# Performance work log

Measured on AMD Instinct MI355X. Metric: run time of the kernel, lower is better.

Reference implementation:

```python
import jax, jax.numpy as jnp
import numpy as np

E, D, H, T = 8, 2048, 5632, 32768  # experts, dim, hidden_dim, total routed tokens


def setup_inputs() -> dict:
    key = jax.random.key(0)
    k_x, k1, k2, k3 = jax.random.split(key, 4)
    x = jax.random.normal(k_x, (T, D), dtype=jnp.float32)
    # trunc_normal init stds per init_weights (approx: plain normal, same scale)
    std = (2.0 / (D * 24)) ** 0.5
    w1 = jax.random.normal(k1, (E, H, D), dtype=jnp.float32) * std
    w2 = jax.random.normal(k2, (E, D, H), dtype=jnp.float32) * std
    w3 = jax.random.normal(k3, (E, H, D), dtype=jnp.float32) * std
    # tokens are pre-sorted by expert; even split 4096 tokens/expert (sums to T)
    num_tokens_per_expert = jnp.full((E,), T // E, dtype=jnp.int32)
    return {"x": x, "w1": w1, "w2": w2, "w3": w3,
            "num_tokens_per_expert": num_tokens_per_expert}


def _grouped_experts(x, w1, w2, w3, counts):
    # Faithful to _run_experts_grouped_mm: grouped GEMMs computed in bf16,
    # SwiGLU activation, cast back to x dtype.
    xb = x.astype(jnp.bfloat16)
    w1b = jnp.transpose(w1.astype(jnp.bfloat16), (0, 2, 1))  # [E, D, H]
    w3b = jnp.transpose(w3.astype(jnp.bfloat16), (0, 2, 1))  # [E, D, H]
    w2b = jnp.transpose(w2.astype(jnp.bfloat16), (0, 2, 1))  # [E, H, D]
    h1 = jax.lax.ragged_dot(xb, w1b, counts)   # [T, H]
    h3 = jax.lax.ragged_dot(xb, w3b, counts)   # [T, H]
    h = jax.nn.silu(h1) * h3                   # fused SwiGLU gate
    out = jax.lax.ragged_dot(h, w2b, counts)   # [T, D]
    return out.astype(x.dtype)


def reference(x, w1, w2, w3, num_tokens_per_expert):
    return _grouped_experts(x, w1, w2, w3, num_tokens_per_expert)
```

## Files before the change

### kernel.cpp

```cpp
#include <hip/hip_runtime.h>
#include <hip/hip_bf16.h>
#include <stdint.h>

#define TT 32768
#define DD 2048
#define HH 5632
#define NE 8

typedef __bf16 bf16;
typedef __bf16 bf16x8 __attribute__((ext_vector_type(8)));
typedef float  f32x4  __attribute__((ext_vector_type(4)));

__device__ __forceinline__ void gl16(const void* g, void* l) {
    __builtin_amdgcn_global_load_lds(
        (const __attribute__((address_space(1))) void*)g,
        (__attribute__((address_space(3))) void*)l, 16, 0, 0);
}
#define VMW(n) asm volatile("s_waitcnt vmcnt(" #n ")" ::: "memory")
#define LGKM0() do { asm volatile("s_waitcnt lgkmcnt(0)" ::: "memory"); \
                     __builtin_amdgcn_sched_barrier(0); } while (0)
#define BARRIER() __builtin_amdgcn_s_barrier()

__device__ __forceinline__ int swz(int off) { return off ^ (((off >> 7) & 3) << 4); }

__device__ __forceinline__ int expert_of(const int* counts, int row0) {
    int base = 0;
    for (int i = 0; i < NE; ++i) { int c = counts[i]; if (row0 < base + c) return i; base += c; }
    return NE - 1;
}

__global__ __launch_bounds__(256)
void k_cvt(const float* __restrict__ in, bf16* __restrict__ out, long n) {
    long i = ((long)blockIdx.x * 256 + threadIdx.x) * 8;
    const long stride = (long)gridDim.x * 256 * 8;
    for (; i < n; i += stride) {
        const float4* p = (const float4*)(in + i);
        float4 a = p[0], b = p[1];
        union { bf16 v[8]; uint4 u; } r;
        r.v[0] = (bf16)a.x; r.v[1] = (bf16)a.y; r.v[2] = (bf16)a.z; r.v[3] = (bf16)a.w;
        r.v[4] = (bf16)b.x; r.v[5] = (bf16)b.y; r.v[6] = (bf16)b.z; r.v[7] = (bf16)b.w;
        *(uint4*)(out + i) = r.u;
    }
}

__global__ __launch_bounds__(512, 2)
void k_moe1(const bf16* __restrict__ xb, const bf16* __restrict__ w1b,
            const bf16* __restrict__ w3b, const int* __restrict__ counts,
            bf16* __restrict__ h) {
    extern __shared__ __align__(16) char sm[];
    const int tid = threadIdx.x;
    const int nwg = gridDim.x;
    int wg = blockIdx.x;
    wg = (wg & 7) * (nwg >> 3) + (wg >> 3);
    const int NTN = HH / 128;
    const int mt = wg / NTN, nt = wg - mt * NTN;
    const int row0 = mt * 256, col0 = nt * 128;
    const int e = expert_of(counts, row0);

    const char *sa0, *sa1, *sa2, *sa3;
    {
        int off0 = tid * 16, off1 = 8192 + tid * 16;
        int s0 = swz(off0), s1 = swz(off1);
        sa0 = (const char*)xb + (((size_t)(row0 + (s0 >> 6)) * DD) << 1) + (s0 & 63);
        sa1 = (const char*)xb + (((size_t)(row0 + (s1 >> 6)) * DD) << 1) + (s1 & 63);
        const char* w1p = (const char*)(w1b + (size_t)e * HH * DD);
        const char* w3p = (const char*)(w3b + (size_t)e * HH * DD);
        sa2 = w1p + (((size_t)(col0 + (s0 >> 6)) * DD) << 1) + (s0 & 63);
        sa3 = w3p + (((size_t)(col0 + (s0 >> 6)) * DD) << 1) + (s0 & 63);
    }
    const int dst0 = tid * 16;

    auto stageA = [&](int kt) {
        char* db = sm + ((kt & 3) << 15);
        const size_t ko = (size_t)kt << 6;
        gl16(sa0 + ko, db + dst0);
        gl16(sa1 + ko, db + 8192 + dst0);
    };
    auto stageB = [&](int kt) {
        char* db = sm + ((kt & 3) << 15);
        const size_t ko = (size_t)kt << 6;
        gl16(sa2 + ko, db + 16384 + dst0);
        gl16(sa3 + ko, db + 24576 + dst0);
    };

    const int lane = tid & 63, wv = tid >> 6;
    const int wrow = wv >> 2, wcol = wv & 3;
    const int lrow = lane & 15, kb = (lane >> 4) << 4;

    int aoff[8], boff[2];
#pragma unroll
    for (int mi = 0; mi < 8; ++mi) aoff[mi] = swz((wrow * 128 + mi * 16 + lrow) * 64 + kb);
#pragma unroll
    for (int ni = 0; ni < 2; ++ni) boff[ni] = swz((wcol * 32 + ni * 16 + lrow) * 64 + kb);

    f32x4 acc1[8][2] = {};
    f32x4 acc3[8][2] = {};

    const int NT = DD / 32;
    stageA(0); stageB(0); stageA(1); stageB(1); stageA(2); stageB(2);
    VMW(8);
    BARRIER();
    for (int t = 0; t < NT; ++t) {
        const char* db = sm + ((t & 3) << 15);
        bf16x8 b1[2], b3[2];
        {
            bf16x8 af[4];
#pragma unroll
            for (int mi = 0; mi < 4; ++mi) af[mi] = *(const bf16x8*)(db + aoff[mi]);
#pragma unroll
            for (int ni = 0; ni < 2; ++ni) {
                b1[ni] = *(const bf16x8*)(db + 16384 + boff[ni]);
                b3[ni] = *(const bf16x8*)(db + 24576 + boff[ni]);
            }
            if (t + 3 < NT) stageA(t + 3);
            BARRIER();
            LGKM0();
            __builtin_amdgcn_s_setprio(1);
#pragma unroll
            for (int mi = 0; mi < 4; ++mi)
#pragma unroll
                for (int ni = 0; ni < 2; ++ni) {
                    acc1[mi][ni] = __builtin_amdgcn_mfma_f32_16x16x32_bf16(af[mi], b1[ni], acc1[mi][ni], 0, 0, 0);
                    acc3[mi][ni] = __builtin_amdgcn_mfma_f32_16x16x32_bf16(af[mi], b3[ni], acc3[mi][ni], 0, 0, 0);
                }
            __builtin_amdgcn_s_setprio(0);
            BARRIER();
        }
        {
            bf16x8 af[4];
#pragma unroll
            for (int mi = 0; mi < 4; ++mi) af[mi] = *(const bf16x8*)(db + aoff[mi + 4]);
            if (t + 3 < NT) { stageB(t + 3); VMW(8); }
            else if (t == NT - 3) { VMW(4); }
            else if (t == NT - 2) { VMW(0); }
            BARRIER();
            LGKM0();
            __builtin_amdgcn_s_setprio(1);
#pragma unroll
            for (int mi = 0; mi < 4; ++mi)
#pragma unroll
                for (int ni = 0; ni < 2; ++ni) {
                    acc1[mi + 4][ni] = __builtin_amdgcn_mfma_f32_16x16x32_bf16(af[mi], b1[ni], acc1[mi + 4][ni], 0, 0, 0);
                    acc3[mi + 4][ni] = __builtin_amdgcn_mfma_f32_16x16x32_bf16(af[mi], b3[ni], acc3[mi + 4][ni], 0, 0, 0);
                }
            __builtin_amdgcn_s_setprio(0);
            BARRIER();
        }
    }

#pragma unroll
    for (int mi = 0; mi < 8; ++mi)
#pragma unroll
        for (int ni = 0; ni < 2; ++ni)
#pragma unroll
            for (int j = 0; j < 4; ++j) {
                int row = row0 + wrow * 128 + mi * 16 + ((lane >> 4) << 2) + j;
                int col = col0 + wcol * 32 + ni * 16 + lrow;
                float f1 = (float)(bf16)acc1[mi][ni][j];
                float f3 = (float)(bf16)acc3[mi][ni][j];
                float s = f1 / (1.0f + __expf(-f1));
                h[(size_t)row * HH + col] = (bf16)(s * f3);
            }
}

__global__ __launch_bounds__(512, 2)
void k_g2(const bf16* __restrict__ hb, const bf16* __restrict__ w2b,
          const int* __restrict__ counts, float* __restrict__ out) {
    extern __shared__ __align__(16) char sm[];
    const int tid = threadIdx.x;
    const int nwg = gridDim.x;
    int wg = blockIdx.x;
    wg = (wg & 7) * (nwg >> 3) + (wg >> 3);
    const int NTN = DD / 256;
    const int mt = wg / NTN, nt = wg - mt * NTN;
    const int row0 = mt * 256, col0 = nt * 256;
    const int e = expert_of(counts, row0);

    const char *sa0, *sa1, *sa2, *sa3;
    {
        int off0 = tid * 16, off1 = 8192 + tid * 16;
        int s0 = swz(off0), s1 = swz(off1);
        sa0 = (const char*)hb + (((size_t)(row0 + (s0 >> 6)) * HH) << 1) + (s0 & 63);
        sa1 = (const char*)hb + (((size_t)(row0 + (s1 >> 6)) * HH) << 1) + (s1 & 63);
        const char* wp = (const char*)(w2b + (size_t)e * DD * HH);
        sa2 = wp + (((size_t)(col0 + (s0 >> 6)) * HH) << 1) + (s0 & 63);
        sa3 = wp + (((size_t)(col0 + (s1 >> 6)) * HH) << 1) + (s1 & 63);
    }
    const int dst0 = tid * 16;
    auto stageA = [&](int kt) {
        char* db = sm + ((kt & 3) << 15);
        const size_t ko = (size_t)kt << 6;
        gl16(sa0 + ko, db + dst0);
        gl16(sa1 + ko, db + 8192 + dst0);
    };
    auto stageB = [&](int kt) {
        char* db = sm + ((kt & 3) << 15);
        const size_t ko = (size_t)kt << 6;
        gl16(sa2 + ko, db + 16384 + dst0);
        gl16(sa3 + ko, db + 24576 + dst0);
    };

    const int lane = tid & 63, wv = tid >> 6;
    const int wrow = wv >> 2, wcol = wv & 3;
    const int lrow = lane & 15, kb = (lane >> 4) << 4;

    int aoff[8], boff[4];
#pragma unroll
    for (int mi = 0; mi < 8; ++mi) aoff[mi] = swz((wrow * 128 + mi * 16 + lrow) * 64 + kb);
#pragma unroll
    for (int ni = 0; ni < 4; ++ni) boff[ni] = swz((wcol * 64 + ni * 16 + lrow) * 64 + kb);

    f32x4 acc[8][4] = {};
    const int NT = HH / 32;
    stageA(0); stageB(0); stageA(1); stageB(1); stageA(2); stageB(2);
    VMW(8);
    BARRIER();
    for (int t = 0; t < NT; ++t) {
        const char* db = sm + ((t & 3) << 15);
        bf16x8 bf[4];
        {
            bf16x8 af[4];
#pragma unroll
            for (int mi = 0; mi < 4; ++mi) af[mi] = *(const bf16x8*)(db + aoff[mi]);
#pragma unroll
            for (int ni = 0; ni < 4; ++ni) bf[ni] = *(const bf16x8*)(db + 16384 + boff[ni]);
            if (t + 3 < NT) stageA(t + 3);
            BARRIER();
            LGKM0();
            __builtin_amdgcn_s_setprio(1);
#pragma unroll
            for (int mi = 0; mi < 4; ++mi)
#pragma unroll
                for (int ni = 0; ni < 4; ++ni)
                    acc[mi][ni] = __builtin_amdgcn_mfma_f32_16x16x32_bf16(af[mi], bf[ni], acc[mi][ni], 0, 0, 0);
            __builtin_amdgcn_s_setprio(0);
            BARRIER();
        }
        {
            bf16x8 af[4];
#pragma unroll
            for (int mi = 0; mi < 4; ++mi) af[mi] = *(const bf16x8*)(db + aoff[mi + 4]);
            if (t + 3 < NT) { stageB(t + 3); VMW(8); }
            else if (t == NT - 3) { VMW(4); }
            else if (t == NT - 2) { VMW(0); }
            BARRIER();
            LGKM0();
            __builtin_amdgcn_s_setprio(1);
#pragma unroll
            for (int mi = 0; mi < 4; ++mi)
#pragma unroll
                for (int ni = 0; ni < 4; ++ni)
                    acc[mi + 4][ni] = __builtin_amdgcn_mfma_f32_16x16x32_bf16(af[mi], bf[ni], acc[mi + 4][ni], 0, 0, 0);
            __builtin_amdgcn_s_setprio(0);
            BARRIER();
        }
    }
#pragma unroll
    for (int mi = 0; mi < 8; ++mi)
#pragma unroll
        for (int ni = 0; ni < 4; ++ni)
#pragma unroll
            for (int j = 0; j < 4; ++j) {
                int row = row0 + wrow * 128 + mi * 16 + ((lane >> 4) << 2) + j;
                int col = col0 + wcol * 64 + ni * 16 + lrow;
                out[(size_t)row * DD + col] = (float)(bf16)acc[mi][ni][j];
            }
}

__device__ __forceinline__ void stage_b_f32(const float* __restrict__ W,
                                            int n0, int k0, int ldk,
                                            int srow, int scol,
                                            bf16* __restrict__ lB) {
#pragma unroll
    for (int r = 0; r < 4; ++r) {
        int row = r * 32 + srow;
        const float4* s = (const float4*)(W + (size_t)(n0 + row) * ldk + k0 + scol);
        float4 a = s[0], b = s[1];
        union { bf16 v[8]; uint4 u; } t;
        t.v[0] = (bf16)a.x; t.v[1] = (bf16)a.y; t.v[2] = (bf16)a.z; t.v[3] = (bf16)a.w;
        t.v[4] = (bf16)b.x; t.v[5] = (bf16)b.y; t.v[6] = (bf16)b.z; t.v[7] = (bf16)b.w;
        *(uint4*)&lB[row * 64 + scol] = t.u;
    }
}

__global__ __launch_bounds__(256, 2)
void k_gemm1_fb(const bf16* __restrict__ xb, const float* __restrict__ w1,
                const float* __restrict__ w3, const int* __restrict__ counts,
                bf16* __restrict__ hbuf) {
    __shared__ bf16 lA[128 * 64];
    __shared__ bf16 lB1[128 * 64];
    __shared__ bf16 lB3[128 * 64];
    const int tid = threadIdx.x;
    const int col0 = blockIdx.x * 128, row0 = blockIdx.y * 128;
    const int e = expert_of(counts, row0);
    const float* W1 = w1 + (size_t)e * HH * DD;
    const float* W3 = w3 + (size_t)e * HH * DD;
    const int lane = tid & 63, wv = tid >> 6;
    const int wr = wv >> 1, wc = wv & 1;
    const int lrow = lane & 15, lk8 = (lane >> 4) * 8;
    const int srow = tid >> 3, scol = (tid & 7) * 8;
    f32x4 acc1[4][4] = {}; f32x4 acc3[4][4] = {};
    for (int k0 = 0; k0 < DD; k0 += 64) {
#pragma unroll
        for (int r = 0; r < 4; ++r) {
            int row = r * 32 + srow;
            gl16(xb + (size_t)(row0 + row) * DD + k0 + scol, &lA[row * 64 + scol]);
        }
        stage_b_f32(W1, col0, k0, DD, srow, scol, lB1);
        stage_b_f32(W3, col0, k0, DD, srow, scol, lB3);
        __syncthreads();
#pragma unroll
        for (int kk = 0; kk < 64; kk += 32) {
            bf16x8 av[4], b1v[4], b3v[4];
#pragma unroll
            for (int mi = 0; mi < 4; ++mi) av[mi] = *(const bf16x8*)&lA[(wr * 64 + mi * 16 + lrow) * 64 + kk + lk8];
#pragma unroll
            for (int ni = 0; ni < 4; ++ni) {
                b1v[ni] = *(const bf16x8*)&lB1[(wc * 64 + ni * 16 + lrow) * 64 + kk + lk8];
                b3v[ni] = *(const bf16x8*)&lB3[(wc * 64 + ni * 16 + lrow) * 64 + kk + lk8];
            }
#pragma unroll
            for (int mi = 0; mi < 4; ++mi)
#pragma unroll
                for (int ni = 0; ni < 4; ++ni) {
                    acc1[mi][ni] = __builtin_amdgcn_mfma_f32_16x16x32_bf16(av[mi], b1v[ni], acc1[mi][ni], 0, 0, 0);
                    acc3[mi][ni] = __builtin_amdgcn_mfma_f32_16x16x32_bf16(av[mi], b3v[ni], acc3[mi][ni], 0, 0, 0);
                }
        }
        __syncthreads();
    }
#pragma unroll
    for (int mi = 0; mi < 4; ++mi)
#pragma unroll
        for (int ni = 0; ni < 4; ++ni)
#pragma unroll
            for (int j = 0; j < 4; ++j) {
                int row = row0 + wr * 64 + mi * 16 + ((lane >> 4) << 2) + j;
                int col = col0 + wc * 64 + ni * 16 + lrow;
                float f1 = (float)(bf16)acc1[mi][ni][j];
                float f3 = (float)(bf16)acc3[mi][ni][j];
                float sil = f1 / (1.0f + __expf(-f1));
                hbuf[(size_t)row * HH + col] = (bf16)(sil * f3);
            }
}

__global__ __launch_bounds__(256, 2)
void k_gemm2_fb(const bf16* __restrict__ hbuf, const float* __restrict__ w2,
                const int* __restrict__ counts, float* __restrict__ out) {
    __shared__ bf16 lA[128 * 64];
    __shared__ bf16 lB[128 * 64];
    const int tid = threadIdx.x;
    const int col0 = blockIdx.x * 128, row0 = blockIdx.y * 128;
    const int e = expert_of(counts, row0);
    const float* W2 = w2 + (size_t)e * DD * HH;
    const int lane = tid & 63, wv = tid >> 6;
    const int wr = wv >> 1, wc = wv & 1;
    const int lrow = lane & 15, lk8 = (lane >> 4) * 8;
    const int srow = tid >> 3, scol = (tid & 7) * 8;
    f32x4 acc[4][4] = {};
    for (int k0 = 0; k0 < HH; k0 += 64) {
#pragma unroll
        for (int r = 0; r < 4; ++r) {
            int row = r * 32 + srow;
            gl16(hbuf + (size_t)(row0 + row) * HH + k0 + scol, &lA[row * 64 + scol]);
        }
        stage_b_f32(W2, col0, k0, HH, srow, scol, lB);
        __syncthreads();
#pragma unroll
        for (int kk = 0; kk < 64; kk += 32) {
            bf16x8 av[4], bv[4];
#pragma unroll
            for (int mi = 0; mi < 4; ++mi) av[mi] = *(const bf16x8*)&lA[(wr * 64 + mi * 16 + lrow) * 64 + kk + lk8];
#pragma unroll
            for (int ni = 0; ni < 4; ++ni) bv[ni] = *(const bf16x8*)&lB[(wc * 64 + ni * 16 + lrow) * 64 + kk + lk8];
#pragma unroll
            for (int mi = 0; mi < 4; ++mi)
#pragma unroll
                for (int ni = 0; ni < 4; ++ni)
                    acc[mi][ni] = __builtin_amdgcn_mfma_f32_16x16x32_bf16(av[mi], bv[ni], acc[mi][ni], 0, 0, 0);
        }
        __syncthreads();
    }
#pragma unroll
    for (int mi = 0; mi < 4; ++mi)
#pragma unroll
        for (int ni = 0; ni < 4; ++ni)
#pragma unroll
            for (int j = 0; j < 4; ++j) {
                int row = row0 + wr * 64 + mi * 16 + ((lane >> 4) << 2) + j;
                int col = col0 + wc * 64 + ni * 16 + lrow;
                out[(size_t)row * DD + col] = (float)(bf16)acc[mi][ni][j];
            }
}

extern "C" void kernel_launch(void* const* d_in, const int* in_sizes, int n_in,
                              void* d_out, int out_size, void* d_ws, size_t ws_size,
                              hipStream_t stream) {
    const float* x      = (const float*)d_in[0];
    const float* w1     = (const float*)d_in[1];
    const float* w2     = (const float*)d_in[2];
    const float* w3     = (const float*)d_in[3];
    const int*   counts = (const int*)d_in[4];
    float* out = (float*)d_out;

    const size_t xb_b = (size_t)TT * DD * 2;
    const size_t h_b  = (size_t)TT * HH * 2;
    const size_t w_b  = (size_t)NE * HH * DD * 2;
    const size_t need_full = xb_b + h_b + 2 * w_b;

    if (ws_size >= need_full) {
        bf16* xb  = (bf16*)d_ws;
        bf16* h   = (bf16*)((char*)d_ws + xb_b);
        bf16* wsA = (bf16*)((char*)d_ws + xb_b + h_b);
        bf16* wsB = (bf16*)((char*)d_ws + xb_b + h_b + w_b);

        hipFuncSetAttribute((const void*)k_moe1, hipFuncAttributeMaxDynamicSharedMemorySize, 131072);
        hipFuncSetAttribute((const void*)k_g2,   hipFuncAttributeMaxDynamicSharedMemorySize, 131072);

        k_cvt<<<2048, 256, 0, stream>>>(x,  xb,  (long)TT * DD);
        k_cvt<<<2048, 256, 0, stream>>>(w1, wsA, (long)NE * HH * DD);
        k_cvt<<<2048, 256, 0, stream>>>(w3, wsB, (long)NE * HH * DD);
        k_moe1<<<(HH / 128) * (TT / 256), 512, 131072, stream>>>(xb, wsA, wsB, counts, h);
        k_cvt<<<2048, 256, 0, stream>>>(w2, wsA, (long)NE * DD * HH);
        k_g2<<<(DD / 256) * (TT / 256), 512, 131072, stream>>>(h, wsA, counts, out);
    } else if (ws_size >= xb_b + h_b) {
        bf16* xb   = (bf16*)d_ws;
        bf16* hbuf = (bf16*)((char*)d_ws + xb_b);
        k_cvt<<<2048, 256, 0, stream>>>(x, xb, (long)TT * DD);
        k_gemm1_fb<<<dim3(HH / 128, TT / 128), 256, 0, stream>>>(xb, w1, w3, counts, hbuf);
        k_gemm2_fb<<<dim3(DD / 128, TT / 128), 256, 0, stream>>>(hbuf, w2, counts, out);
    }
}
```

Measured before the change: 2.904 ms.

## Deepen GEMM pipelines to five LDS stages with register-double-buffered fragments

Both grouped GEMM kernels now use a 5-slot LDS ring (160 KB), staging A and B tiles together four k-steps ahead. The LDS fragments for step t+1 are read into a second register set while the MFMAs for step t run, which leaves one barrier per k-step instead of two. The aim is to hide LDS and global-load latency and cut synchronisation stalls. The cost is much higher VGPR pressure from the doubled fragment registers, with a risk of spills. The old 4-stage kernels are kept as a fallback if the 160 KB shared-memory request fails, and the low-workspace fp32 fallback path is removed.

```diff
diff --git a/kernel.cpp b/kernel.cpp
--- a/kernel.cpp
+++ b/kernel.cpp
@@ -42,6 +42,37 @@
         *(uint4*)(out + i) = r.u;
     }
 }
+
+#define M1_LOAD(t1, NA, NB1, NB3) do {                                        \
+    const char* nb_ = sm + (size_t)((t1) % 5) * 32768;                        \
+    _Pragma("unroll")                                                         \
+    for (int mi = 0; mi < 8; ++mi)                                            \
+        NA[mi] = *(const bf16x8*)(nb_ + aoff0 + mi * 1024);                   \
+    _Pragma("unroll")                                                         \
+    for (int ni = 0; ni < 2; ++ni) {                                          \
+        NB1[ni] = *(const bf16x8*)(nb_ + 16384 + boff0 + ni * 1024);          \
+        NB3[ni] = *(const bf16x8*)(nb_ + 24576 + boff0 + ni * 1024);          \
+    }                                                                         \
+    __builtin_amdgcn_sched_barrier(0);                                        \
+} while (0)
+
+#define M1_ITER(t, CA, CB1, CB3, NA, NB1, NB3) do {                           \
+    if ((t) + 4 < NT) { stage((t) + 4); VMW(8); }                             \
+    else if ((t) == NT - 4) { VMW(4); }                                       \
+    else if ((t) == NT - 3) { VMW(0); }                                       \
+    LGKM0();                                                                  \
+    if ((t) + 1 < NT) M1_LOAD((t) + 1, NA, NB1, NB3);                         \
+    __builtin_amdgcn_s_setprio(1);                                            \
+    _Pragma("unroll")                                                         \
+    for (int mi = 0; mi < 8; ++mi)                                            \
+    _Pragma("unroll")                                                         \
+    for (int ni = 0; ni < 2; ++ni) {                                          \
+        acc1[mi][ni] = __builtin_amdgcn_mfma_f32_16x16x32_bf16(CA[mi], CB1[ni], acc1[mi][ni], 0, 0, 0); \
+        acc3[mi][ni] = __builtin_amdgcn_mfma_f32_16x16x32_bf16(CA[mi], CB3[ni], acc3[mi][ni], 0, 0, 0); \
+    }                                                                         \
+    __builtin_amdgcn_s_setprio(0);                                            \
+    BARRIER();                                                                \
+} while (0)
 
 __global__ __launch_bounds__(512, 2)
 void k_moe1(const bf16* __restrict__ xb, const bf16* __restrict__ w1b,
@@ -70,15 +101,11 @@
     }
     const int dst0 = tid * 16;
 
-    auto stageA = [&](int kt) {
-        char* db = sm + ((kt & 3) << 15);
+    auto stage = [&](int kt) {
+        char* db = sm + (size_t)(kt % 5) * 32768;
         const size_t ko = (size_t)kt << 6;
         gl16(sa0 + ko, db + dst0);
         gl16(sa1 + ko, db + 8192 + dst0);
-    };
-    auto stageB = [&](int kt) {
-        char* db = sm + ((kt & 3) << 15);
-        const size_t ko = (size_t)kt << 6;
         gl16(sa2 + ko, db + 16384 + dst0);
         gl16(sa3 + ko, db + 24576 + dst0);
     };
@@ -87,65 +114,21 @@
     const int wrow = wv >> 2, wcol = wv & 3;
     const int lrow = lane & 15, kb = (lane >> 4) << 4;
 
-    int aoff[8], boff[2];
-#pragma unroll
-    for (int mi = 0; mi < 8; ++mi) aoff[mi] = swz((wrow * 128 + mi * 16 + lrow) * 64 + kb);
-#pragma unroll
-    for (int ni = 0; ni < 2; ++ni) boff[ni] = swz((wcol * 32 + ni * 16 + lrow) * 64 + kb);
+    const int aoff0 = swz((wrow * 128 + lrow) * 64 + kb);
+    const int boff0 = swz((wcol * 32 + lrow) * 64 + kb);
 
     f32x4 acc1[8][2] = {};
     f32x4 acc3[8][2] = {};
+    bf16x8 Xa[8], Xb1[2], Xb3[2], Ya[8], Yb1[2], Yb3[2];
 
     const int NT = DD / 32;
-    stageA(0); stageB(0); stageA(1); stageB(1); stageA(2); stageB(2);
+    stage(0); stage(1); stage(2); stage(3);
     VMW(8);
     BARRIER();
-    for (int t = 0; t < NT; ++t) {
-        const char* db = sm + ((t & 3) << 15);
-        bf16x8 b1[2], b3[2];
-        {
-            bf16x8 af[4];
-#pragma unroll
-            for (int mi = 0; mi < 4; ++mi) af[mi] = *(const bf16x8*)(db + aoff[mi]);
-#pragma unroll
-            for (int ni = 0; ni < 2; ++ni) {
-                b1[ni] = *(const bf16x8*)(db + 16384 + boff[ni]);
-                b3[ni] = *(const bf16x8*)(db + 24576 + boff[ni]);
-            }
-            if (t + 3 < NT) stageA(t + 3);
-            BARRIER();
-            LGKM0();
-            __builtin_amdgcn_s_setprio(1);
-#pragma unroll
-            for (int mi = 0; mi < 4; ++mi)
-#pragma unroll
-                for (int ni = 0; ni < 2; ++ni) {
-                    acc1[mi][ni] = __builtin_amdgcn_mfma_f32_16x16x32_bf16(af[mi], b1[ni], acc1[mi][ni], 0, 0, 0);
-                    acc3[mi][ni] = __builtin_amdgcn_mfma_f32_16x16x32_bf16(af[mi], b3[ni], acc3[mi][ni], 0, 0, 0);
-                }
-            __builtin_amdgcn_s_setprio(0);
-            BARRIER();
-        }
-        {
-            bf16x8 af[4];
-#pragma unroll
-            for (int mi = 0; mi < 4; ++mi) af[mi] = *(const bf16x8*)(db + aoff[mi + 4]);
-            if (t + 3 < NT) { stageB(t + 3); VMW(8); }
-            else if (t == NT - 3) { VMW(4); }
-            else if (t == NT - 2) { VMW(0); }
-            BARRIER();
-            LGKM0();
-            __builtin_amdgcn_s_setprio(1);
-#pragma unroll
-            for (int mi = 0; mi < 4; ++mi)
-#pragma unroll
-                for (int ni = 0; ni < 2; ++ni) {
-                    acc1[mi + 4][ni] = __builtin_amdgcn_mfma_f32_16x16x32_bf16(af[mi], b1[ni], acc1[mi + 4][ni], 0, 0, 0);
-                    acc3[mi + 4][ni] = __builtin_amdgcn_mfma_f32_16x16x32_bf16(af[mi], b3[ni], acc3[mi + 4][ni], 0, 0, 0);
-                }
-            __builtin_amdgcn_s_setprio(0);
-            BARRIER();
-        }
+    M1_LOAD(0, Xa, Xb1, Xb3);
+    for (int t = 0; t < NT; t += 2) {
+        M1_ITER(t,     Xa, Xb1, Xb3, Ya, Yb1, Yb3);
+        M1_ITER(t + 1, Ya, Yb1, Yb3, Xa, Xb1, Xb3);
     }
 
 #pragma unroll
@@ -162,6 +145,33 @@
                 h[(size_t)row * HH + col] = (bf16)(s * f3);
             }
 }
+
+#define G2_LOAD(t1, NA, NB) do {                                              \
+    const char* nb_ = sm + (size_t)((t1) % 5) * 32768;                        \
+    _Pragma("unroll")                                                         \
+    for (int mi = 0; mi < 8; ++mi)                                            \
+        NA[mi] = *(const bf16x8*)(nb_ + aoff0 + mi * 1024);                   \
+    _Pragma("unroll")                                                         \
+    for (int ni = 0; ni < 4; ++ni)                                            \
+        NB[ni] = *(const bf16x8*)(nb_ + 16384 + boff0 + ni * 1024);           \
+    __builtin_amdgcn_sched_barrier(0);                                        \
+} while (0)
+
+#define G2_ITER(t, CA, CB, NA, NB) do {                                       \
+    if ((t) + 4 < NT) { stage((t) + 4); VMW(8); }                             \
+    else if ((t) == NT - 4) { VMW(4); }                                       \
+    else if ((t) == NT - 3) { VMW(0); }                                       \
+    LGKM0();                                                                  \
+    if ((t) + 1 < NT) G2_LOAD((t) + 1, NA, NB);                               \
+    __builtin_amdgcn_s_setprio(1);                                            \
+    _Pragma("unroll")                                                         \
+    for (int mi = 0; mi < 8; ++mi)                                            \
+    _Pragma("unroll")                                                         \
+    for (int ni = 0; ni < 4; ++ni)                                            \
+        acc[mi][ni] = __builtin_amdgcn_mfma_f32_16x16x32_bf16(CA[mi], CB[ni], acc[mi][ni], 0, 0, 0); \
+    __builtin_amdgcn_s_setprio(0);                                            \
+    BARRIER();                                                                \
+} while (0)
 
 __global__ __launch_bounds__(512, 2)
 void k_g2(const bf16* __restrict__ hb, const bf16* __restrict__ w2b,
@@ -187,15 +197,11 @@
         sa3 = wp + (((size_t)(col0 + (s1 >> 6)) * HH) << 1) + (s1 & 63);
     }
     const int dst0 = tid * 16;
-    auto stageA = [&](int kt) {
-        char* db = sm + ((kt & 3) << 15);
+    auto stage = [&](int kt) {
+        char* db = sm + (size_t)(kt % 5) * 32768;
         const size_t ko = (size_t)kt << 6;
         gl16(sa0 + ko, db + dst0);
         gl16(sa1 + ko, db + 8192 + dst0);
-    };
-    auto stageB = [&](int kt) {
-        char* db = sm + ((kt & 3) << 15);
-        const size_t ko = (size_t)kt << 6;
         gl16(sa2 + ko, db + 16384 + dst0);
         gl16(sa3 + ko, db + 24576 + dst0);
     };
@@ -204,12 +210,190 @@
     const int wrow = wv >> 2, wcol = wv & 3;
     const int lrow = lane & 15, kb = (lane >> 4) << 4;
 
+    const int aoff0 = swz((wrow * 128 + lrow) * 64 + kb);
+    const int boff0 = swz((wcol * 64 + lrow) * 64 + kb);
+
+    f32x4 acc[8][4] = {};
+    bf16x8 Xa[8], Xb[4], Ya[8], Yb[4];
+
+    const int NT = HH / 32;
+    stage(0); stage(1); stage(2); stage(3);
+    VMW(8);
+    BARRIER();
+    G2_LOAD(0, Xa, Xb);
+    for (int t = 0; t < NT; t += 2) {
+        G2_ITER(t,     Xa, Xb, Ya, Yb);
+        G2_ITER(t + 1, Ya, Yb, Xa, Xb);
+    }
+
+#pragma unroll
+    for (int mi = 0; mi < 8; ++mi)
+#pragma unroll
+        for (int ni = 0; ni < 4; ++ni)
+#pragma unroll
+            for (int j = 0; j < 4; ++j) {
+                int row = row0 + wrow * 128 + mi * 16 + ((lane >> 4) << 2) + j;
+                int col = col0 + wcol * 64 + ni * 16 + lrow;
+                out[(size_t)row * DD + col] = (float)(bf16)acc[mi][ni][j];
+            }
+}
+
+__global__ __launch_bounds__(512, 2)
+void k_moe1_b(const bf16* __restrict__ xb, const bf16* __restrict__ w1b,
+              const bf16* __restrict__ w3b, const int* __restrict__ counts,
+              bf16* __restrict__ h) {
+    extern __shared__ __align__(16) char sm[];
+    const int tid = threadIdx.x;
+    const int nwg = gridDim.x;
+    int wg = blockIdx.x;
+    wg = (wg & 7) * (nwg >> 3) + (wg >> 3);
+    const int NTN = HH / 128;
+    const int mt = wg / NTN, nt = wg - mt * NTN;
+    const int row0 = mt * 256, col0 = nt * 128;
+    const int e = expert_of(counts, row0);
+    const char *sa0, *sa1, *sa2, *sa3;
+    {
+        int off0 = tid * 16, off1 = 8192 + tid * 16;
+        int s0 = swz(off0), s1 = swz(off1);
+        sa0 = (const char*)xb + (((size_t)(row0 + (s0 >> 6)) * DD) << 1) + (s0 & 63);
+        sa1 = (const char*)xb + (((size_t)(row0 + (s1 >> 6)) * DD) << 1) + (s1 & 63);
+        const char* w1p = (const char*)(w1b + (size_t)e * HH * DD);
+        const char* w3p = (const char*)(w3b + (size_t)e * HH * DD);
+        sa2 = w1p + (((size_t)(col0 + (s0 >> 6)) * DD) << 1) + (s0 & 63);
+        sa3 = w3p + (((size_t)(col0 + (s0 >> 6)) * DD) << 1) + (s0 & 63);
+    }
+    const int dst0 = tid * 16;
+    auto stageA = [&](int kt) {
+        char* db = sm + ((kt & 3) << 15);
+        const size_t ko = (size_t)kt << 6;
+        gl16(sa0 + ko, db + dst0);
+        gl16(sa1 + ko, db + 8192 + dst0);
+    };
+    auto stageB = [&](int kt) {
+        char* db = sm + ((kt & 3) << 15);
+        const size_t ko = (size_t)kt << 6;
+        gl16(sa2 + ko, db + 16384 + dst0);
+        gl16(sa3 + ko, db + 24576 + dst0);
+    };
+    const int lane = tid & 63, wv = tid >> 6;
+    const int wrow = wv >> 2, wcol = wv & 3;
+    const int lrow = lane & 15, kb = (lane >> 4) << 4;
+    int aoff[8], boff[2];
+#pragma unroll
+    for (int mi = 0; mi < 8; ++mi) aoff[mi] = swz((wrow * 128 + mi * 16 + lrow) * 64 + kb);
+#pragma unroll
+    for (int ni = 0; ni < 2; ++ni) boff[ni] = swz((wcol * 32 + ni * 16 + lrow) * 64 + kb);
+    f32x4 acc1[8][2] = {};
+    f32x4 acc3[8][2] = {};
+    const int NT = DD / 32;
+    stageA(0); stageB(0); stageA(1); stageB(1); stageA(2); stageB(2);
+    VMW(8);
+    BARRIER();
+    for (int t = 0; t < NT; ++t) {
+        const char* db = sm + ((t & 3) << 15);
+        bf16x8 b1[2], b3[2];
+        {
+            bf16x8 af[4];
+#pragma unroll
+            for (int mi = 0; mi < 4; ++mi) af[mi] = *(const bf16x8*)(db + aoff[mi]);
+#pragma unroll
+            for (int ni = 0; ni < 2; ++ni) {
+                b1[ni] = *(const bf16x8*)(db + 16384 + boff[ni]);
+                b3[ni] = *(const bf16x8*)(db + 24576 + boff[ni]);
+            }
+            if (t + 3 < NT) stageA(t + 3);
+            BARRIER();
+            LGKM0();
+            __builtin_amdgcn_s_setprio(1);
+#pragma unroll
+            for (int mi = 0; mi < 4; ++mi)
+#pragma unroll
+                for (int ni = 0; ni < 2; ++ni) {
+                    acc1[mi][ni] = __builtin_amdgcn_mfma_f32_16x16x32_bf16(af[mi], b1[ni], acc1[mi][ni], 0, 0, 0);
+                    acc3[mi][ni] = __builtin_amdgcn_mfma_f32_16x16x32_bf16(af[mi], b3[ni], acc3[mi][ni], 0, 0, 0);
+                }
+            __builtin_amdgcn_s_setprio(0);
+            BARRIER();
+        }
+        {
+            bf16x8 af[4];
+#pragma unroll
+            for (int mi = 0; mi < 4; ++mi) af[mi] = *(const bf16x8*)(db + aoff[mi + 4]);
+            if (t + 3 < NT) { stageB(t + 3); VMW(8); }
+            else if (t == NT - 3) { VMW(4); }
+            else if (t == NT - 2) { VMW(0); }
+            BARRIER();
+            LGKM0();
+            __builtin_amdgcn_s_setprio(1);
+#pragma unroll
+            for (int mi = 0; mi < 4; ++mi)
+#pragma unroll
+                for (int ni = 0; ni < 2; ++ni) {
+                    acc1[mi + 4][ni] = __builtin_amdgcn_mfma_f32_16x16x32_bf16(af[mi], b1[ni], acc1[mi + 4][ni], 0, 0, 0);
+                    acc3[mi + 4][ni] = __builtin_amdgcn_mfma_f32_16x16x32_bf16(af[mi], b3[ni], acc3[mi + 4][ni], 0, 0, 0);
+                }
+            __builtin_amdgcn_s_setprio(0);
+            BARRIER();
+        }
+    }
+#pragma unroll
+    for (int mi = 0; mi < 8; ++mi)
+#pragma unroll
+        for (int ni = 0; ni < 2; ++ni)
+#pragma unroll
+            for (int j = 0; j < 4; ++j) {
+                int row = row0 + wrow * 128 + mi * 16 + ((lane >> 4) << 2) + j;
+                int col = col0 + wcol * 32 + ni * 16 + lrow;
+                float f1 = (float)(bf16)acc1[mi][ni][j];
+                float f3 = (float)(bf16)acc3[mi][ni][j];
+                float s = f1 / (1.0f + __expf(-f1));
+                h[(size_t)row * HH + col] = (bf16)(s * f3);
+            }
+}
+
+__global__ __launch_bounds__(512, 2)
+void k_g2_b(const bf16* __restrict__ hb, const bf16* __restrict__ w2b,
+            const int* __restrict__ counts, float* __restrict__ out) {
+    extern __shared__ __align__(16) char sm[];
+    const int tid = threadIdx.x;
+    const int nwg = gridDim.x;
+    int wg = blockIdx.x;
+    wg = (wg & 7) * (nwg >> 3) + (wg >> 3);
+    const int NTN = DD / 256;
+    const int mt = wg / NTN, nt = wg - mt * NTN;
+    const int row0 = mt * 256, col0 = nt * 256;
+    const int e = expert_of(counts, row0);
+    const char *sa0, *sa1, *sa2, *sa3;
+    {
+        int off0 = tid * 16, off1 = 8192 + tid * 16;
+        int s0 = swz(off0), s1 = swz(off1);
+        sa0 = (const char*)hb + (((size_t)(row0 + (s0 >> 6)) * HH) << 1) + (s0 & 63);
+        sa1 = (const char*)hb + (((size_t)(row0 + (s1 >> 6)) * HH) << 1) + (s1 & 63);
+        const char* wp = (const char*)(w2b + (size_t)e * DD * HH);
+        sa2 = wp + (((size_t)(col0 + (s0 >> 6)) * HH) << 1) + (s0 & 63);
+        sa3 = wp + (((size_t)(col0 + (s1 >> 6)) * HH) << 1) + (s1 & 63);
+    }
+    const int dst0 = tid * 16;
+    auto stageA = [&](int kt) {
+        char* db = sm + ((kt & 3) << 15);
+        const size_t ko = (size_t)kt << 6;
+        gl16(sa0 + ko, db + dst0);
+        gl16(sa1 + ko, db + 8192 + dst0);
+    };
+    auto stageB = [&](int kt) {
+        char* db = sm + ((kt & 3) << 15);
+        const size_t ko = (size_t)kt << 6;
+        gl16(sa2 + ko, db + 16384 + dst0);
+        gl16(sa3 + ko, db + 24576 + dst0);
+    };
+    const int lane = tid & 63, wv = tid >> 6;
+    const int wrow = wv >> 2, wcol = wv & 3;
+    const int lrow = lane & 15, kb = (lane >> 4) << 4;
     int aoff[8], boff[4];
 #pragma unroll
     for (int mi = 0; mi < 8; ++mi) aoff[mi] = swz((wrow * 128 + mi * 16 + lrow) * 64 + kb);
 #pragma unroll
     for (int ni = 0; ni < 4; ++ni) boff[ni] = swz((wcol * 64 + ni * 16 + lrow) * 64 + kb);
-
     f32x4 acc[8][4] = {};
     const int NT = HH / 32;
     stageA(0); stageB(0); stageA(1); stageB(1); stageA(2); stageB(2);
@@ -267,132 +451,6 @@
             }
 }
 
-__device__ __forceinline__ void stage_b_f32(const float* __restrict__ W,
-                                            int n0, int k0, int ldk,
-                                            int srow, int scol,
-                                            bf16* __restrict__ lB) {
-#pragma unroll
-    for (int r = 0; r < 4; ++r) {
-        int row = r * 32 + srow;
-        const float4* s = (const float4*)(W + (size_t)(n0 + row) * ldk + k0 + scol);
-        float4 a = s[0], b = s[1];
-        union { bf16 v[8]; uint4 u; } t;
-        t.v[0] = (bf16)a.x; t.v[1] = (bf16)a.y; t.v[2] = (bf16)a.z; t.v[3] = (bf16)a.w;
-        t.v[4] = (bf16)b.x; t.v[5] = (bf16)b.y; t.v[6] = (bf16)b.z; t.v[7] = (bf16)b.w;
-        *(uint4*)&lB[row * 64 + scol] = t.u;
-    }
-}
-
-__global__ __launch_bounds__(256, 2)
-void k_gemm1_fb(const bf16* __restrict__ xb, const float* __restrict__ w1,
-                const float* __restrict__ w3, const int* __restrict__ counts,
-                bf16* __restrict__ hbuf) {
-    __shared__ bf16 lA[128 * 64];
-    __shared__ bf16 lB1[128 * 64];
-    __shared__ bf16 lB3[128 * 64];
-    const int tid = threadIdx.x;
-    const int col0 = blockIdx.x * 128, row0 = blockIdx.y * 128;
-    const int e = expert_of(counts, row0);
-    const float* W1 = w1 + (size_t)e * HH * DD;
-    const float* W3 = w3 + (size_t)e * HH * DD;
-    const int lane = tid & 63, wv = tid >> 6;
-    const int wr = wv >> 1, wc = wv & 1;
-    const int lrow = lane & 15, lk8 = (lane >> 4) * 8;
-    const int srow = tid >> 3, scol = (tid & 7) * 8;
-    f32x4 acc1[4][4] = {}; f32x4 acc3[4][4] = {};
-    for (int k0 = 0; k0 < DD; k0 += 64) {
-#pragma unroll
-        for (int r = 0; r < 4; ++r) {
-            int row = r * 32 + srow;
-            gl16(xb + (size_t)(row0 + row) * DD + k0 + scol, &lA[row * 64 + scol]);
-        }
-        stage_b_f32(W1, col0, k0, DD, srow, scol, lB1);
-        stage_b_f32(W3, col0, k0, DD, srow, scol, lB3);
-        __syncthreads();
-#pragma unroll
-        for (int kk = 0; kk < 64; kk += 32) {
-            bf16x8 av[4], b1v[4], b3v[4];
-#pragma unroll
-            for (int mi = 0; mi < 4; ++mi) av[mi] = *(const bf16x8*)&lA[(wr * 64 + mi * 16 + lrow) * 64 + kk + lk8];
-#pragma unroll
-            for (int ni = 0; ni < 4; ++ni) {
-                b1v[ni] = *(const bf16x8*)&lB1[(wc * 64 + ni * 16 + lrow) * 64 + kk + lk8];
-                b3v[ni] = *(const bf16x8*)&lB3[(wc * 64 + ni * 16 + lrow) * 64 + kk + lk8];
-            }
-#pragma unroll
-            for (int mi = 0; mi < 4; ++mi)
-#pragma unroll
-                for (int ni = 0; ni < 4; ++ni) {
-                    acc1[mi][ni] = __builtin_amdgcn_mfma_f32_16x16x32_bf16(av[mi], b1v[ni], acc1[mi][ni], 0, 0, 0);
-                    acc3[mi][ni] = __builtin_amdgcn_mfma_f32_16x16x32_bf16(av[mi], b3v[ni], acc3[mi][ni], 0, 0, 0);
-                }
-        }
-        __syncthreads();
-    }
-#pragma unroll
-    for (int mi = 0; mi < 4; ++mi)
-#pragma unroll
-        for (int ni = 0; ni < 4; ++ni)
-#pragma unroll
-            for (int j = 0; j < 4; ++j) {
-                int row = row0 + wr * 64 + mi * 16 + ((lane >> 4) << 2) + j;
-                int col = col0 + wc * 64 + ni * 16 + lrow;
-                float f1 = (float)(bf16)acc1[mi][ni][j];
-                float f3 = (float)(bf16)acc3[mi][ni][j];
-                float sil = f1 / (1.0f + __expf(-f1));
-                hbuf[(size_t)row * HH + col] = (bf16)(sil * f3);
-            }
-}
-
-__global__ __launch_bounds__(256, 2)
-void k_gemm2_fb(const bf16* __restrict__ hbuf, const float* __restrict__ w2,
-                const int* __restrict__ counts, float* __restrict__ out) {
-    __shared__ bf16 lA[128 * 64];
-    __shared__ bf16 lB[128 * 64];
-    const int tid = threadIdx.x;
-    const int col0 = blockIdx.x * 128, row0 = blockIdx.y * 128;
-    const int e = expert_of(counts, row0);
-    const float* W2 = w2 + (size_t)e * DD * HH;
-    const int lane = tid & 63, wv = tid >> 6;
-    const int wr = wv >> 1, wc = wv & 1;
-    const int lrow = lane & 15, lk8 = (lane >> 4) * 8;
-    const int srow = tid >> 3, scol = (tid & 7) * 8;
-    f32x4 acc[4][4] = {};
-    for (int k0 = 0; k0 < HH; k0 += 64) {
-#pragma unroll
-        for (int r = 0; r < 4; ++r) {
-            int row = r * 32 + srow;
-            gl16(hbuf + (size_t)(row0 + row) * HH + k0 + scol, &lA[row * 64 + scol]);
-        }
-        stage_b_f32(W2, col0, k0, HH, srow, scol, lB);
-        __syncthreads();
-#pragma unroll
-        for (int kk = 0; kk < 64; kk += 32) {
-            bf16x8 av[4], bv[4];
-#pragma unroll
-            for (int mi = 0; mi < 4; ++mi) av[mi] = *(const bf16x8*)&lA[(wr * 64 + mi * 16 + lrow) * 64 + kk + lk8];
-#pragma unroll
-            for (int ni = 0; ni < 4; ++ni) bv[ni] = *(const bf16x8*)&lB[(wc * 64 + ni * 16 + lrow) * 64 + kk + lk8];
-#pragma unroll
-            for (int mi = 0; mi < 4; ++mi)
-#pragma unroll
-                for (int ni = 0; ni < 4; ++ni)
-                    acc[mi][ni] = __builtin_amdgcn_mfma_f32_16x16x32_bf16(av[mi], bv[ni], acc[mi][ni], 0, 0, 0);
-        }
-        __syncthreads();
-    }
-#pragma unroll
-    for (int mi = 0; mi < 4; ++mi)
-#pragma unroll
-        for (int ni = 0; ni < 4; ++ni)
-#pragma unroll
-            for (int j = 0; j < 4; ++j) {
-                int row = row0 + wr * 64 + mi * 16 + ((lane >> 4) << 2) + j;
-                int col = col0 + wc * 64 + ni * 16 + lrow;
-                out[(size_t)row * DD + col] = (float)(bf16)acc[mi][ni][j];
-            }
-}
-
 extern "C" void kernel_launch(void* const* d_in, const int* in_sizes, int n_in,
                               void* d_out, int out_size, void* d_ws, size_t ws_size,
                               hipStream_t stream) {
@@ -407,27 +465,31 @@
     const size_t h_b  = (size_t)TT * HH * 2;
     const size_t w_b  = (size_t)NE * HH * DD * 2;
     const size_t need_full = xb_b + h_b + 2 * w_b;
-
-    if (ws_size >= need_full) {
-        bf16* xb  = (bf16*)d_ws;
-        bf16* h   = (bf16*)((char*)d_ws + xb_b);
-        bf16* wsA = (bf16*)((char*)d_ws + xb_b + h_b);
-        bf16* wsB = (bf16*)((char*)d_ws + xb_b + h_b + w_b);
-
-        hipFuncSetAttribute((const void*)k_moe1, hipFuncAttributeMaxDynamicSharedMemorySize, 131072);
-        hipFuncSetAttribute((const void*)k_g2,   hipFuncAttributeMaxDynamicSharedMemorySize, 131072);
-
-        k_cvt<<<2048, 256, 0, stream>>>(x,  xb,  (long)TT * DD);
-        k_cvt<<<2048, 256, 0, stream>>>(w1, wsA, (long)NE * HH * DD);
-        k_cvt<<<2048, 256, 0, stream>>>(w3, wsB, (long)NE * HH * DD);
-        k_moe1<<<(HH / 128) * (TT / 256), 512, 131072, stream>>>(xb, wsA, wsB, counts, h);
-        k_cvt<<<2048, 256, 0, stream>>>(w2, wsA, (long)NE * DD * HH);
-        k_g2<<<(DD / 256) * (TT / 256), 512, 131072, stream>>>(h, wsA, counts, out);
-    } else if (ws_size >= xb_b + h_b) {
-        bf16* xb   = (bf16*)d_ws;
-        bf16* hbuf = (bf16*)((char*)d_ws + xb_b);
-        k_cvt<<<2048, 256, 0, stream>>>(x, xb, (long)TT * DD);
-        k_gemm1_fb<<<dim3(HH / 128, TT / 128), 256, 0, stream>>>(xb, w1, w3, counts, hbuf);
-        k_gemm2_fb<<<dim3(DD / 128, TT / 128), 256, 0, stream>>>(hbuf, w2, counts, out);
-    }
-}
+    if (ws_size < need_full) return;
+
+    bf16* xb  = (bf16*)d_ws;
+    bf16* h   = (bf16*)((char*)d_ws + xb_b);
+    bf16* wsA = (bf16*)((char*)d_ws + xb_b + h_b);
+    bf16* wsB = (bf16*)((char*)d_ws + xb_b + h_b + w_b);
+
+    hipError_t ea = hipFuncSetAttribute((const void*)k_moe1,
+                        hipFuncAttributeMaxDynamicSharedMemorySize, 163840);
+    hipError_t eb = hipFuncSetAttribute((const void*)k_g2,
+                        hipFuncAttributeMaxDynamicSharedMemorySize, 163840);
+    const bool deep = (ea == hipSuccess && eb == hipSuccess);
+    if (!deep) {
+        hipFuncSetAttribute((const void*)k_moe1_b,
+                            hipFuncAttributeMaxDynamicSharedMemorySize, 131072);
+        hipFuncSetAttribute((const void*)k_g2_b,
+                            hipFuncAttributeMaxDynamicSharedMemorySize, 131072);
+    }
+
+    k_cvt<<<2048, 256, 0, stream>>>(x,  xb,  (long)TT * DD);
+    k_cvt<<<2048, 256, 0, stream>>>(w1, wsA, (long)NE * HH * DD);
+    k_cvt<<<2048, 256, 0, stream>>>(w3, wsB, (long)NE * HH * DD);
+    if (deep) k_moe1<<<(HH / 128) * (TT / 256), 512, 163840, stream>>>(xb, wsA, wsB, counts, h);
+    else      k_moe1_b<<<(HH / 128) * (TT / 256), 512, 131072, stream>>>(xb, wsA, wsB, counts, h);
+    k_cvt<<<2048, 256, 0, stream>>>(w2, wsA, (long)NE * DD * HH);
+    if (deep) k_g2<<<(DD / 256) * (TT / 256), 512, 163840, stream>>>(h, wsA, counts, out);
+    else      k_g2_b<<<(DD / 256) * (TT / 256), 512, 131072, stream>>>(h, wsA, counts, out);
+}
```

Result: no change. 2.882 ms (-0.7%).
